# Kernel tuning notes

Hardware: AMD Instinct MI355X
Metric: run time of the kernel (lower is better)

## Reference

```python
import jax, jax.numpy as jnp
import numpy as np

HID = 1024
HEADS = 16
DH = HID // HEADS
SCALE = DH ** -0.5
L, B = 2048, 2


def setup_inputs() -> dict:
    key = jax.random.key(0)
    ks = jax.random.split(key, 16)
    inp = {
        "query": jax.random.normal(ks[0], (L, B, HID), jnp.float32),
        "key": jax.random.normal(ks[1], (L, B, HID), jnp.float32),
        "value": jax.random.normal(ks[2], (L, B, HID), jnp.float32),
        "mask": jax.random.randint(ks[3], (B, L), 0, 2).astype(bool),
    }
    # xavier-uniform linear weights (torch Linear stores [out, in]; y = x @ W.T + b)
    lim = (6.0 / (HID + HID)) ** 0.5
    for i, name in enumerate(["wq", "wk", "wv", "wfc"]):
        inp[name] = jax.random.uniform(ks[4 + i], (HID, HID), jnp.float32, -lim, lim)
    inp["bq"] = jnp.zeros((HID,), jnp.float32)
    inp["bk"] = jnp.zeros((HID,), jnp.float32)
    inp["bv"] = jnp.zeros((HID,), jnp.float32)
    inp["bfc"] = jnp.zeros((HID,), jnp.float32)
    inp["tao"] = jnp.full((HEADS,), 10.0, jnp.float32)
    return inp


def reference(query, key, value, mask, wq, bq, wk, bk, wv, bv, wfc, bfc, tao):
    # inputs arrive [L, B, D]; module transposes to [B, L, D]
    q = jnp.swapaxes(query, 0, 1)
    k = jnp.swapaxes(key, 0, 1)
    v = jnp.swapaxes(value, 0, 1)
    bsz, length, _ = q.shape

    def heads(x, w, b):
        y = x @ w.T + b                      # [B, L, D]
        return y.reshape(bsz, length, HEADS, DH).transpose(0, 2, 1, 3)  # [B, H, L, d]

    Q = heads(q, wq, bq)
    K = heads(k, wk, bk)
    V = heads(v, wv, bv)

    qk = jnp.einsum("bhqd,bhkd->bhqk", Q, K) * SCALE  # [B, H, L, L]

    # gaussian positional bias: -|i-j|^2/2 * tao_h^-4
    idx = jnp.arange(length, dtype=jnp.float32)
    dist = -0.5 * (idx[:, None] - idx[None, :]) ** 2          # [L, L]
    qk = qk + dist[None, None, :, :] * (tao ** -4)[None, :, None, None]

    qk = jnp.where(mask[:, None, None, :], -jnp.inf, qk)
    attn = jax.nn.softmax(qk, axis=-1)  # dropout is identity in eval mode

    x = jnp.einsum("bhqk,bhkd->bhqd", attn, V)            # [B, H, L, d]
    x = x.transpose(0, 2, 1, 3).reshape(bsz, length, HID)  # [B, L, D]
    x = x @ wfc.T + bfc
    return jnp.swapaxes(x, 0, 1)  # [L, B, D]
```

## Files before the change

kernel.cpp:

```cpp
#include <hip/hip_runtime.h>

#define LQ   2048
#define BQ   2
#define HID  1024
#define NH   16
#define DH   64
#define SCALE 0.125f
#define L2E  1.44269504088896f
#define C1   0.18033688011f
#define EXPOFF 23.0831206542f

using short8  = __attribute__((ext_vector_type(8))) short;
using ushort8 = __attribute__((ext_vector_type(8))) unsigned short;
using f32x4   = __attribute__((ext_vector_type(4))) float;
typedef unsigned short u16;
typedef __attribute__((ext_vector_type(2))) __bf16 bf16x2;

__device__ inline u16 f2bf(float x) {
    unsigned int u = __float_as_uint(x);
    u = (u + 0x7fffu + ((u >> 16) & 1u)) >> 16;
    return (u16)u;
}

#if defined(__has_builtin)
#if __has_builtin(__builtin_amdgcn_cvt_pk_bf16_f32)
#define HAVE_PKBF 1
#endif
#if __has_builtin(__builtin_amdgcn_exp2f)
#define HAVE_EXP2 1
#endif
#endif

__device__ inline unsigned int pkbf(float a, float b) {
#ifdef HAVE_PKBF
    bf16x2 r = __builtin_amdgcn_cvt_pk_bf16_f32(a, b);
    return __builtin_bit_cast(unsigned int, r);
#else
    return (unsigned int)f2bf(a) | ((unsigned int)f2bf(b) << 16);
#endif
}

__device__ inline float fexp2(float x) {
#ifdef HAVE_EXP2
    return __builtin_amdgcn_exp2f(x);
#else
    return exp2f(x);
#endif
}

__device__ inline void gl_lds16(const void* g, void* l) {
    __builtin_amdgcn_global_load_lds(
        (const __attribute__((address_space(1))) void*)g,
        (__attribute__((address_space(3))) void*)l, 16, 0, 0);
}

struct CastArgs {
    const float* s[7];
    u16* d[7];
    int n[7];
    const unsigned char* mraw;
    int* mout;
    int mn;
};

__global__ __launch_bounds__(256) void castw(CastArgs a) {
    const int y = blockIdx.y;
    const int t = threadIdx.x;
    if (y == 7) {
        if (blockIdx.x != 0) return;
        __shared__ int cnt;
        if (t == 0) cnt = 0;
        __syncthreads();
        int local = 0;
        for (int i = t; i < a.mn; i += 256)
            if ((i & 3) && a.mraw[i]) local++;
        atomicAdd(&cnt, local);
        __syncthreads();
        bool isInt32 = (cnt == 0);
        const int* mi = (const int*)a.mraw;
        for (int i = t; i < a.mn; i += 256)
            a.mout[i] = isInt32 ? mi[i] : (int)a.mraw[i];
        return;
    }
    const float* s = a.s[y];
    u16* d = a.d[y];
    const int n4 = a.n[y] >> 2;
    for (int i = blockIdx.x * 256 + t; i < n4; i += gridDim.x * 256) {
        float4 v = *(const float4*)(s + (size_t)i * 4);
        uint2 p;
        p.x = pkbf(v.x, v.y);
        p.y = pkbf(v.z, v.w);
        *(uint2*)(d + (size_t)i * 4) = p;
    }
}

struct QkvArgs {
    const u16* A[3];
    const u16* W[3];
    const float* bias[3];
    u16* out[3];
};

__global__ __launch_bounds__(256) void gemm_qkv(QkvArgs ga) {
    __shared__ u16 As[128][64];
    __shared__ u16 Bs[128][64];

    const int z = blockIdx.z;
    const u16* A = ga.A[z];
    const u16* W = ga.W[z];
    const float* bias = ga.bias[z];
    u16* outp = ga.out[z];

    const int t = threadIdx.x;
    const int m0 = blockIdx.x * 128;
    const int n0 = blockIdx.y * 128;
    const int lane = t & 63;
    const int lane15 = lane & 15;
    const int quad = lane >> 4;
    const int w = t >> 6;
    const int wm = (w >> 1) * 64;
    const int wn = (w & 1) * 64;

    const int lrow = lane >> 3;
    const int ch = (lane & 7) ^ ((lane >> 3) & 7);
    const u16* aS = A + (size_t)(m0 + 32 * w + lrow) * HID + 8 * ch;
    const u16* bS = W + (size_t)(n0 + 32 * w + lrow) * HID + 8 * ch;

    const int s0 = (quad ^ (lane15 & 7)) * 8;
    const int s1 = ((4 + quad) ^ (lane15 & 7)) * 8;

    f32x4 acc[4][4];
#pragma unroll
    for (int i = 0; i < 4; i++)
#pragma unroll
        for (int j = 0; j < 4; j++) acc[i][j] = (f32x4){0,0,0,0};

    for (int k0 = 0; k0 < HID; k0 += 64) {
        __syncthreads();
#pragma unroll
        for (int i = 0; i < 4; i++) {
            gl_lds16(aS + (size_t)(8 * i) * HID + k0, &As[32 * w + 8 * i][0]);
            gl_lds16(bS + (size_t)(8 * i) * HID + k0, &Bs[32 * w + 8 * i][0]);
        }
        __syncthreads();

        short8 af0[4], af1[4], bf0[4], bf1[4];
#pragma unroll
        for (int i = 0; i < 4; i++) {
            const u16* ar = &As[wm + i * 16 + lane15][0];
            const u16* br = &Bs[wn + i * 16 + lane15][0];
            af0[i] = *(const short8*)(ar + s0);
            af1[i] = *(const short8*)(ar + s1);
            bf0[i] = *(const short8*)(br + s0);
            bf1[i] = *(const short8*)(br + s1);
        }
#pragma unroll
        for (int mi = 0; mi < 4; mi++)
#pragma unroll
            for (int ni = 0; ni < 4; ni++) {
                acc[mi][ni] = __builtin_amdgcn_mfma_f32_16x16x32_bf16(af0[mi], bf0[ni], acc[mi][ni], 0, 0, 0);
                acc[mi][ni] = __builtin_amdgcn_mfma_f32_16x16x32_bf16(af1[mi], bf1[ni], acc[mi][ni], 0, 0, 0);
            }
    }

#pragma unroll
    for (int mi = 0; mi < 4; mi++) {
#pragma unroll
        for (int ni = 0; ni < 4; ni++) {
            const int n = n0 + wn + ni * 16 + lane15;
            const float bv = bias[n];
            const int h = n >> 6, d = n & 63;
#pragma unroll
            for (int r = 0; r < 4; r++) {
                const int m = m0 + wm + mi * 16 + quad * 4 + r;
                const float c = acc[mi][ni][r] + bv;
                const int b = m & 1, l = m >> 1;
                if (z < 2) {
                    outp[(((size_t)(b * NH + h)) * LQ + l) * DH + d] = f2bf(c);
                } else {
                    outp[(((size_t)(b * NH + h)) * DH + d) * LQ + l] = f2bf(c);
                }
            }
        }
    }
}

__global__ __launch_bounds__(256) void gemm_fc(const u16* __restrict__ A,
                                               const u16* __restrict__ W,
                                               const float* __restrict__ bias,
                                               float* __restrict__ outp) {
    __shared__ u16 As[128][64];
    __shared__ u16 Bs[64][64];

    const int t = threadIdx.x;
    const int m0 = blockIdx.x * 128;
    const int n0 = blockIdx.y * 64;
    const int lane = t & 63;
    const int lane15 = lane & 15;
    const int quad = lane >> 4;
    const int w = t >> 6;
    const int wm = (w >> 1) * 64;
    const int wn = (w & 1) * 32;

    const int lrow = lane >> 3;
    const int ch = (lane & 7) ^ ((lane >> 3) & 7);
    const u16* aS = A + (size_t)(m0 + 32 * w + lrow) * HID + 8 * ch;
    const u16* bS = W + (size_t)(n0 + 16 * w + lrow) * HID + 8 * ch;

    const int s0 = (quad ^ (lane15 & 7)) * 8;
    const int s1 = ((4 + quad) ^ (lane15 & 7)) * 8;

    f32x4 acc[4][2];
#pragma unroll
    for (int i = 0; i < 4; i++)
#pragma unroll
        for (int j = 0; j < 2; j++) acc[i][j] = (f32x4){0,0,0,0};

    for (int k0 = 0; k0 < HID; k0 += 64) {
        __syncthreads();
#pragma unroll
        for (int i = 0; i < 4; i++)
            gl_lds16(aS + (size_t)(8 * i) * HID + k0, &As[32 * w + 8 * i][0]);
#pragma unroll
        for (int i = 0; i < 2; i++)
            gl_lds16(bS + (size_t)(8 * i) * HID + k0, &Bs[16 * w + 8 * i][0]);
        __syncthreads();

        short8 af0[4], af1[4], bf0[2], bf1[2];
#pragma unroll
        for (int i = 0; i < 4; i++) {
            const u16* ar = &As[wm + i * 16 + lane15][0];
            af0[i] = *(const short8*)(ar + s0);
            af1[i] = *(const short8*)(ar + s1);
        }
#pragma unroll
        for (int j = 0; j < 2; j++) {
            const u16* br = &Bs[wn + j * 16 + lane15][0];
            bf0[j] = *(const short8*)(br + s0);
            bf1[j] = *(const short8*)(br + s1);
        }
#pragma unroll
        for (int mi = 0; mi < 4; mi++)
#pragma unroll
            for (int ni = 0; ni < 2; ni++) {
                acc[mi][ni] = __builtin_amdgcn_mfma_f32_16x16x32_bf16(af0[mi], bf0[ni], acc[mi][ni], 0, 0, 0);
                acc[mi][ni] = __builtin_amdgcn_mfma_f32_16x16x32_bf16(af1[mi], bf1[ni], acc[mi][ni], 0, 0, 0);
            }
    }

#pragma unroll
    for (int mi = 0; mi < 4; mi++) {
#pragma unroll
        for (int ni = 0; ni < 2; ni++) {
            const int n = n0 + wn + ni * 16 + lane15;
            const float bv = bias[n];
#pragma unroll
            for (int r = 0; r < 4; r++) {
                const int m = m0 + wm + mi * 16 + quad * 4 + r;
                outp[(size_t)m * HID + n] = acc[mi][ni][r] + bv;
            }
        }
    }
}

#define PSTR 72

__global__ __launch_bounds__(512) void attn_kernel(const u16* __restrict__ Qg,
                                                   const u16* __restrict__ Kg,
                                                   const u16* __restrict__ Vtg,
                                                   const int* __restrict__ maskI,
                                                   const float* __restrict__ tao,
                                                   u16* __restrict__ Xa) {
    __shared__ u16 Ks[128][64];
    __shared__ u16 Vt[64][128];
    __shared__ u16 PT[128][PSTR];
    __shared__ float smask[128];

    const int bh = blockIdx.x;
    const int q0 = blockIdx.y * 128;
    const int b = bh >> 4;
    const int h = bh & 15;
    const int t = threadIdx.x;
    const int w = t >> 6;
    const int lane = t & 63;
    const int lane15 = lane & 15;
    const int quad = lane >> 4;

    const u16* Kbase = Kg + (size_t)bh * LQ * DH;
    const u16* Vtbase = Vtg + (size_t)bh * DH * LQ;
    const int* mrow = maskI + b * LQ;

    const float tv = tao[h];
    const float t2 = tv * tv;
    const float nb = -0.5f / (t2 * t2);
    const float nb2 = nb * L2E;
    const float skipd2 = -40.0f / nb2;

    const int qrow = q0 + w * 16 + lane15;
    short8 qB0, qB1;
    {
        const u16* qp_ = Qg + ((size_t)bh * LQ + qrow) * DH + quad * 8;
        qB0 = *(const short8*)(qp_);
        qB1 = *(const short8*)(qp_ + 32);
    }

    const int krow = 8 * w + (lane >> 3);
    const int kch = (lane & 7) ^ ((lane >> 3) & 7);
    const u16* kS = Kbase + (size_t)krow * DH + 8 * kch;
    const int vrow = 4 * w + (lane >> 4);
    const int vch = (lane & 8) | ((lane & 7) ^ (vrow & 7));
    const u16* vS = Vtbase + (size_t)vrow * LQ + 8 * vch;
    u16* kD0 = &Ks[8 * w][0];
    u16* kD1 = &Ks[64 + 8 * w][0];
    u16* vD0 = &Vt[4 * w][0];
    u16* vD1 = &Vt[32 + 4 * w][0];

    const int s0 = (quad ^ (lane15 & 7)) * 8;
    const int s1 = ((4 + quad) ^ (lane15 & 7)) * 8;

    f32x4 O[4];
#pragma unroll
    for (int mt = 0; mt < 4; mt++) O[mt] = (f32x4){0,0,0,0};
    float l_ = 0.0f;

    const float ebase0 = (float)(qrow - quad * 4);
    const int prow = w * 16 + lane15;

    for (int k0 = 0; k0 < LQ; k0 += 128) {
        {
            int dmin = 0;
            if (k0 > q0 + 127) dmin = k0 - (q0 + 127);
            else if (k0 + 127 < q0) dmin = q0 - (k0 + 127);
            const float df = (float)dmin;
            if (df * df > skipd2) continue;
        }
        __syncthreads();
        gl_lds16(kS + (size_t)k0 * DH, kD0);
        gl_lds16(kS + (size_t)(k0 + 64) * DH, kD1);
        gl_lds16(vS + k0, vD0);
        gl_lds16(vS + (size_t)32 * LQ + k0, vD1);
        if (t < 128) smask[t] = mrow[k0 + t] ? -3.0e38f : -EXPOFF;
        __syncthreads();

#pragma unroll
        for (int hh = 0; hh < 2; hh++) {
            const int kbase = 64 * hh;
            f32x4 S[4];
#pragma unroll
            for (int kt = 0; kt < 4; kt++) {
                const u16* kr = &Ks[kbase + kt * 16 + lane15][0];
                const short8 ka = *(const short8*)(kr + s0);
                const short8 kb = *(const short8*)(kr + s1);
                S[kt] = __builtin_amdgcn_mfma_f32_16x16x32_bf16(ka, qB0, (f32x4){0,0,0,0}, 0, 0, 0);
                S[kt] = __builtin_amdgcn_mfma_f32_16x16x32_bf16(kb, qB1, S[kt], 0, 0, 0);
            }

            const float ebase = ebase0 - (float)(k0 + kbase);
            float lacc = 0.0f;
#pragma unroll
            for (int kt = 0; kt < 4; kt++) {
                const float4 sm4 = *(const float4*)&smask[kbase + kt * 16 + quad * 4];
                float p[4];
#pragma unroll
                for (int r = 0; r < 4; r++) {
                    const float d = ebase - (float)(kt * 16 + r);
                    const float tb = fmaf(nb2 * d, d, ((const float*)&sm4)[r]);
                    p[r] = fexp2(fmaf(S[kt][r], C1, tb));
                    lacc += p[r];
                }
                uint2 pk2;
                pk2.x = pkbf(p[0], p[1]);
                pk2.y = pkbf(p[2], p[3]);
                *(uint2*)&PT[prow][kt * 16 + quad * 4] = pk2;
            }
            l_ += lacc;

            const short8 pB0 = *(const short8*)&PT[prow][quad * 8];
            const short8 pB1 = *(const short8*)&PT[prow][32 + quad * 8];
#pragma unroll
            for (int mt = 0; mt < 4; mt++) {
                const u16* vr = &Vt[mt * 16 + lane15][kbase];
                const short8 va = *(const short8*)(vr + s0);
                const short8 vb = *(const short8*)(vr + s1);
                O[mt] = __builtin_amdgcn_mfma_f32_16x16x32_bf16(va, pB0, O[mt], 0, 0, 0);
                O[mt] = __builtin_amdgcn_mfma_f32_16x16x32_bf16(vb, pB1, O[mt], 0, 0, 0);
            }
        }
    }

    l_ += __shfl_xor(l_, 16, 64);
    l_ += __shfl_xor(l_, 32, 64);

    {
        const float inv = 1.0f / l_;
        u16* dst = Xa + ((size_t)qrow * BQ + b) * HID + h * DH;
#pragma unroll
        for (int mt = 0; mt < 4; mt++) {
            uint2 pk2;
            pk2.x = pkbf(O[mt][0] * inv, O[mt][1] * inv);
            pk2.y = pkbf(O[mt][2] * inv, O[mt][3] * inv);
            *(uint2*)(dst + mt * 16 + quad * 4) = pk2;
        }
    }
}

extern "C" void kernel_launch(void* const* d_in, const int* in_sizes, int n_in,
                              void* d_out, int out_size, void* d_ws, size_t ws_size,
                              hipStream_t stream) {
    const float* q    = (const float*)d_in[0];
    const float* k    = (const float*)d_in[1];
    const float* v    = (const float*)d_in[2];
    const void*  mask = d_in[3];
    const float* wq   = (const float*)d_in[4];
    const float* wk   = (const float*)d_in[5];
    const float* wv   = (const float*)d_in[6];
    const float* wfc  = (const float*)d_in[7];
    const float* bq   = (const float*)d_in[8];
    const float* bk   = (const float*)d_in[9];
    const float* bv   = (const float*)d_in[10];
    const float* bfc  = (const float*)d_in[11];
    const float* tao  = (const float*)d_in[12];

    const size_t NE = (size_t)LQ * BQ * HID;
    const size_t NW = (size_t)HID * HID;
    u16* base = (u16*)d_ws;
    u16* Qp    = base;
    u16* Kp    = base + NE;
    u16* Vtp   = base + 2 * NE;
    u16* Xa    = base + 3 * NE;
    u16* qbf   = base + 4 * NE;
    u16* kbf   = base + 5 * NE;
    u16* vbf   = base + 6 * NE;
    u16* wqbf  = base + 7 * NE;
    u16* wkbf  = wqbf + NW;
    u16* wvbf  = wkbf + NW;
    u16* wfcbf = wvbf + NW;
    int* maskI = (int*)(wfcbf + NW);

    CastArgs ca;
    ca.s[0] = q;   ca.d[0] = qbf;   ca.n[0] = (int)NE;
    ca.s[1] = k;   ca.d[1] = kbf;   ca.n[1] = (int)NE;
    ca.s[2] = v;   ca.d[2] = vbf;   ca.n[2] = (int)NE;
    ca.s[3] = wq;  ca.d[3] = wqbf;  ca.n[3] = (int)NW;
    ca.s[4] = wk;  ca.d[4] = wkbf;  ca.n[4] = (int)NW;
    ca.s[5] = wv;  ca.d[5] = wvbf;  ca.n[5] = (int)NW;
    ca.s[6] = wfc; ca.d[6] = wfcbf; ca.n[6] = (int)NW;
    ca.mraw = (const unsigned char*)mask;
    ca.mout = maskI;
    ca.mn = BQ * LQ;
    castw<<<dim3(256, 8), 256, 0, stream>>>(ca);

    QkvArgs ga;
    ga.A[0] = qbf;  ga.W[0] = wqbf;  ga.bias[0] = bq;  ga.out[0] = Qp;
    ga.A[1] = kbf;  ga.W[1] = wkbf;  ga.bias[1] = bk;  ga.out[1] = Kp;
    ga.A[2] = vbf;  ga.W[2] = wvbf;  ga.bias[2] = bv;  ga.out[2] = Vtp;
    gemm_qkv<<<dim3(32, 8, 3), 256, 0, stream>>>(ga);

    attn_kernel<<<dim3(32, 16), 512, 0, stream>>>(Qp, Kp, Vtp, maskI, tao, Xa);

    gemm_fc<<<dim3(32, 16), 256, 0, stream>>>(Xa, wfcbf, bfc, (float*)d_out);
}
```

Baseline: 233.1 us.

## Swap MFMA operand order for vectorized packed epilogue stores in QKV and FC GEMMs

The QKV GEMM shrinks its tile to 128x64 and doubles the grid. It swaps MFMA A/B operands so each lane holds four contiguous output columns, which lets the epilogue write packed bf16 pairs (uint2) and float4 instead of scalar strided stores. For the V projection, input rows are remapped so that consecutive M rows map to consecutive sequence positions, giving contiguous stores into the transposed Vt layout. The FC GEMM gets the same operand swap and float4 output stores. The smaller tile reduces per-block reuse in exchange for more blocks and cheaper epilogue writes.

Result: no change. 236.5 us (+1.4%).

```diff
diff --git a/kernel.cpp b/kernel.cpp
--- a/kernel.cpp
+++ b/kernel.cpp
@@ -102,95 +102,14 @@
 };
 
 __global__ __launch_bounds__(256) void gemm_qkv(QkvArgs ga) {
-    __shared__ u16 As[128][64];
-    __shared__ u16 Bs[128][64];
+    __shared__ u16 Xs[128][64];
+    __shared__ u16 Ws[64][64];
 
     const int z = blockIdx.z;
-    const u16* A = ga.A[z];
-    const u16* W = ga.W[z];
+    const u16* Xg = ga.A[z];
+    const u16* Wg = ga.W[z];
     const float* bias = ga.bias[z];
     u16* outp = ga.out[z];
-
-    const int t = threadIdx.x;
-    const int m0 = blockIdx.x * 128;
-    const int n0 = blockIdx.y * 128;
-    const int lane = t & 63;
-    const int lane15 = lane & 15;
-    const int quad = lane >> 4;
-    const int w = t >> 6;
-    const int wm = (w >> 1) * 64;
-    const int wn = (w & 1) * 64;
-
-    const int lrow = lane >> 3;
-    const int ch = (lane & 7) ^ ((lane >> 3) & 7);
-    const u16* aS = A + (size_t)(m0 + 32 * w + lrow) * HID + 8 * ch;
-    const u16* bS = W + (size_t)(n0 + 32 * w + lrow) * HID + 8 * ch;
-
-    const int s0 = (quad ^ (lane15 & 7)) * 8;
-    const int s1 = ((4 + quad) ^ (lane15 & 7)) * 8;
-
-    f32x4 acc[4][4];
-#pragma unroll
-    for (int i = 0; i < 4; i++)
-#pragma unroll
-        for (int j = 0; j < 4; j++) acc[i][j] = (f32x4){0,0,0,0};
-
-    for (int k0 = 0; k0 < HID; k0 += 64) {
-        __syncthreads();
-#pragma unroll
-        for (int i = 0; i < 4; i++) {
-            gl_lds16(aS + (size_t)(8 * i) * HID + k0, &As[32 * w + 8 * i][0]);
-            gl_lds16(bS + (size_t)(8 * i) * HID + k0, &Bs[32 * w + 8 * i][0]);
-        }
-        __syncthreads();
-
-        short8 af0[4], af1[4], bf0[4], bf1[4];
-#pragma unroll
-        for (int i = 0; i < 4; i++) {
-            const u16* ar = &As[wm + i * 16 + lane15][0];
-            const u16* br = &Bs[wn + i * 16 + lane15][0];
-            af0[i] = *(const short8*)(ar + s0);
-            af1[i] = *(const short8*)(ar + s1);
-            bf0[i] = *(const short8*)(br + s0);
-            bf1[i] = *(const short8*)(br + s1);
-        }
-#pragma unroll
-        for (int mi = 0; mi < 4; mi++)
-#pragma unroll
-            for (int ni = 0; ni < 4; ni++) {
-                acc[mi][ni] = __builtin_amdgcn_mfma_f32_16x16x32_bf16(af0[mi], bf0[ni], acc[mi][ni], 0, 0, 0);
-                acc[mi][ni] = __builtin_amdgcn_mfma_f32_16x16x32_bf16(af1[mi], bf1[ni], acc[mi][ni], 0, 0, 0);
-            }
-    }
-
-#pragma unroll
-    for (int mi = 0; mi < 4; mi++) {
-#pragma unroll
-        for (int ni = 0; ni < 4; ni++) {
-            const int n = n0 + wn + ni * 16 + lane15;
-            const float bv = bias[n];
-            const int h = n >> 6, d = n & 63;
-#pragma unroll
-            for (int r = 0; r < 4; r++) {
-                const int m = m0 + wm + mi * 16 + quad * 4 + r;
-                const float c = acc[mi][ni][r] + bv;
-                const int b = m & 1, l = m >> 1;
-                if (z < 2) {
-                    outp[(((size_t)(b * NH + h)) * LQ + l) * DH + d] = f2bf(c);
-                } else {
-                    outp[(((size_t)(b * NH + h)) * DH + d) * LQ + l] = f2bf(c);
-                }
-            }
-        }
-    }
-}
-
-__global__ __launch_bounds__(256) void gemm_fc(const u16* __restrict__ A,
-                                               const u16* __restrict__ W,
-                                               const float* __restrict__ bias,
-                                               float* __restrict__ outp) {
-    __shared__ u16 As[128][64];
-    __shared__ u16 Bs[64][64];
 
     const int t = threadIdx.x;
     const int m0 = blockIdx.x * 128;
@@ -199,8 +118,125 @@
     const int lane15 = lane & 15;
     const int quad = lane >> 4;
     const int w = t >> 6;
-    const int wm = (w >> 1) * 64;
-    const int wn = (w & 1) * 32;
+    const int mw = (w & 1) * 64;
+    const int nw = (w >> 1) * 32;
+
+    const int lrow = lane >> 3;
+    const int ch = (lane & 7) ^ ((lane >> 3) & 7);
+
+    const int xrow0 = m0 + 32 * w + lrow;
+    const u16* wS = Wg + (size_t)(n0 + 16 * w + lrow) * HID + 8 * ch;
+
+    const int s0 = (quad ^ (lane15 & 7)) * 8;
+    const int s1 = ((4 + quad) ^ (lane15 & 7)) * 8;
+
+    f32x4 acc[8];
+#pragma unroll
+    for (int i = 0; i < 8; i++) acc[i] = (f32x4){0,0,0,0};
+
+    const u16* xS[4];
+#pragma unroll
+    for (int i = 0; i < 4; i++) {
+        int mrow = xrow0 + 8 * i;
+        int g = (z < 2) ? mrow : (2 * (mrow & 2047) + (mrow >> 11));
+        xS[i] = Xg + (size_t)g * HID + 8 * ch;
+    }
+
+    for (int k0 = 0; k0 < HID; k0 += 64) {
+        __syncthreads();
+#pragma unroll
+        for (int i = 0; i < 4; i++)
+            gl_lds16(xS[i] + k0, &Xs[32 * w + 8 * i][0]);
+#pragma unroll
+        for (int i = 0; i < 2; i++)
+            gl_lds16(wS + (size_t)(8 * i) * HID + k0, &Ws[16 * w + 8 * i][0]);
+        __syncthreads();
+
+        short8 xa0[4], xa1[4], wb0[2], wb1[2];
+#pragma unroll
+        for (int i = 0; i < 4; i++) {
+            const u16* xr = &Xs[mw + i * 16 + lane15][0];
+            xa0[i] = *(const short8*)(xr + s0);
+            xa1[i] = *(const short8*)(xr + s1);
+        }
+#pragma unroll
+        for (int j = 0; j < 2; j++) {
+            const u16* wr = &Ws[nw + j * 16 + lane15][0];
+            wb0[j] = *(const short8*)(wr + s0);
+            wb1[j] = *(const short8*)(wr + s1);
+        }
+        if (z < 2) {
+#pragma unroll
+            for (int ni = 0; ni < 2; ni++)
+#pragma unroll
+                for (int mi = 0; mi < 4; mi++) {
+                    acc[ni * 4 + mi] = __builtin_amdgcn_mfma_f32_16x16x32_bf16(wb0[ni], xa0[mi], acc[ni * 4 + mi], 0, 0, 0);
+                    acc[ni * 4 + mi] = __builtin_amdgcn_mfma_f32_16x16x32_bf16(wb1[ni], xa1[mi], acc[ni * 4 + mi], 0, 0, 0);
+                }
+        } else {
+#pragma unroll
+            for (int ni = 0; ni < 2; ni++)
+#pragma unroll
+                for (int mi = 0; mi < 4; mi++) {
+                    acc[ni * 4 + mi] = __builtin_amdgcn_mfma_f32_16x16x32_bf16(xa0[mi], wb0[ni], acc[ni * 4 + mi], 0, 0, 0);
+                    acc[ni * 4 + mi] = __builtin_amdgcn_mfma_f32_16x16x32_bf16(xa1[mi], wb1[ni], acc[ni * 4 + mi], 0, 0, 0);
+                }
+        }
+    }
+
+    const int h = n0 >> 6;
+    if (z < 2) {
+#pragma unroll
+        for (int ni = 0; ni < 2; ni++) {
+#pragma unroll
+            for (int mi = 0; mi < 4; mi++) {
+                const int m = m0 + mw + mi * 16 + lane15;
+                const int b = m & 1, l = m >> 1;
+                const int d = nw + ni * 16 + quad * 4;
+                const f32x4 a = acc[ni * 4 + mi];
+                const float4 bv = *(const float4*)&bias[n0 + d];
+                uint2 pk2;
+                pk2.x = pkbf(a[0] + bv.x, a[1] + bv.y);
+                pk2.y = pkbf(a[2] + bv.z, a[3] + bv.w);
+                *(uint2*)&outp[(((size_t)(b * NH + h)) * LQ + l) * DH + d] = pk2;
+            }
+        }
+    } else {
+#pragma unroll
+        for (int ni = 0; ni < 2; ni++) {
+#pragma unroll
+            for (int mi = 0; mi < 4; mi++) {
+                const int mp = m0 + mw + mi * 16 + quad * 4;
+                const int b = mp >> 11;
+                const int l = mp & 2047;
+                const int d = nw + ni * 16 + lane15;
+                const float bv = bias[n0 + d];
+                const f32x4 a = acc[ni * 4 + mi];
+                uint2 pk2;
+                pk2.x = pkbf(a[0] + bv, a[1] + bv);
+                pk2.y = pkbf(a[2] + bv, a[3] + bv);
+                *(uint2*)&outp[(((size_t)(b * NH + h)) * DH + d) * LQ + l] = pk2;
+            }
+        }
+    }
+}
+
+__global__ __launch_bounds__(256) void gemm_fc(const u16* __restrict__ A,
+                                               const u16* __restrict__ W,
+                                               const float* __restrict__ bias,
+                                               float* __restrict__ outp) {
+    __shared__ u16 As[128][64];
+    __shared__ u16 Bs[64][64];
+
+    const int t = threadIdx.x;
+    const int m0 = blockIdx.x * 128;
+    const int n0 = blockIdx.y * 64;
+    const int lane = t & 63;
+    const int lane15 = lane & 15;
+    const int quad = lane >> 4;
+    const int w = t >> 6;
+    const int mw = (w & 1) * 64;
+    const int nw = (w >> 1) * 32;
 
     const int lrow = lane >> 3;
     const int ch = (lane & 7) ^ ((lane >> 3) & 7);
@@ -210,11 +246,9 @@
     const int s0 = (quad ^ (lane15 & 7)) * 8;
     const int s1 = ((4 + quad) ^ (lane15 & 7)) * 8;
 
-    f32x4 acc[4][2];
-#pragma unroll
-    for (int i = 0; i < 4; i++)
-#pragma unroll
-        for (int j = 0; j < 2; j++) acc[i][j] = (f32x4){0,0,0,0};
+    f32x4 acc[8];
+#pragma unroll
+    for (int i = 0; i < 8; i++) acc[i] = (f32x4){0,0,0,0};
 
     for (int k0 = 0; k0 < HID; k0 += 64) {
         __syncthreads();
@@ -226,39 +260,40 @@
             gl_lds16(bS + (size_t)(8 * i) * HID + k0, &Bs[16 * w + 8 * i][0]);
         __syncthreads();
 
-        short8 af0[4], af1[4], bf0[2], bf1[2];
+        short8 xa0[4], xa1[4], wb0[2], wb1[2];
 #pragma unroll
         for (int i = 0; i < 4; i++) {
-            const u16* ar = &As[wm + i * 16 + lane15][0];
-            af0[i] = *(const short8*)(ar + s0);
-            af1[i] = *(const short8*)(ar + s1);
+            const u16* ar = &As[mw + i * 16 + lane15][0];
+            xa0[i] = *(const short8*)(ar + s0);
+            xa1[i] = *(const short8*)(ar + s1);
         }
 #pragma unroll
         for (int j = 0; j < 2; j++) {
-            const u16* br = &Bs[wn + j * 16 + lane15][0];
-            bf0[j] = *(const short8*)(br + s0);
-            bf1[j] = *(const short8*)(br + s1);
-        }
-#pragma unroll
-        for (int mi = 0; mi < 4; mi++)
-#pragma unroll
-            for (int ni = 0; ni < 2; ni++) {
-                acc[mi][ni] = __builtin_amdgcn_mfma_f32_16x16x32_bf16(af0[mi], bf0[ni], acc[mi][ni], 0, 0, 0);
-                acc[mi][ni] = __builtin_amdgcn_mfma_f32_16x16x32_bf16(af1[mi], bf1[ni], acc[mi][ni], 0, 0, 0);
-            }
-    }
-
-#pragma unroll
-    for (int mi = 0; mi < 4; mi++) {
-#pragma unroll
-        for (int ni = 0; ni < 2; ni++) {
-            const int n = n0 + wn + ni * 16 + lane15;
-            const float bv = bias[n];
-#pragma unroll
-            for (int r = 0; r < 4; r++) {
-                const int m = m0 + wm + mi * 16 + quad * 4 + r;
-                outp[(size_t)m * HID + n] = acc[mi][ni][r] + bv;
-            }
+            const u16* br = &Bs[nw + j * 16 + lane15][0];
+            wb0[j] = *(const short8*)(br + s0);
+            wb1[j] = *(const short8*)(br + s1);
+        }
+#pragma unroll
+        for (int ni = 0; ni < 2; ni++)
+#pragma unroll
+            for (int mi = 0; mi < 4; mi++) {
+                acc[ni * 4 + mi] = __builtin_amdgcn_mfma_f32_16x16x32_bf16(wb0[ni], xa0[mi], acc[ni * 4 + mi], 0, 0, 0);
+                acc[ni * 4 + mi] = __builtin_amdgcn_mfma_f32_16x16x32_bf16(wb1[ni], xa1[mi], acc[ni * 4 + mi], 0, 0, 0);
+            }
+    }
+
+#pragma unroll
+    for (int ni = 0; ni < 2; ni++) {
+#pragma unroll
+        for (int mi = 0; mi < 4; mi++) {
+            const int m = m0 + mw + mi * 16 + lane15;
+            const int n = n0 + nw + ni * 16 + quad * 4;
+            const float4 bv = *(const float4*)&bias[n];
+            const f32x4 a = acc[ni * 4 + mi];
+            float4 o;
+            o.x = a[0] + bv.x; o.y = a[1] + bv.y;
+            o.z = a[2] + bv.z; o.w = a[3] + bv.w;
+            *(float4*)&outp[(size_t)m * HID + n] = o;
         }
     }
 }
@@ -454,7 +489,7 @@
     ga.A[0] = qbf;  ga.W[0] = wqbf;  ga.bias[0] = bq;  ga.out[0] = Qp;
     ga.A[1] = kbf;  ga.W[1] = wkbf;  ga.bias[1] = bk;  ga.out[1] = Kp;
     ga.A[2] = vbf;  ga.W[2] = wvbf;  ga.bias[2] = bv;  ga.out[2] = Vtp;
-    gemm_qkv<<<dim3(32, 8, 3), 256, 0, stream>>>(ga);
+    gemm_qkv<<<dim3(32, 16, 3), 256, 0, stream>>>(ga);
 
     attn_kernel<<<dim3(32, 16), 512, 0, stream>>>(Qp, Kp, Vtp, maskI, tao, Xa);
 
```
